# Optimization experiments

Hardware: AMD Instinct MI355X
Metric: run time of the kernel (lower is better)

## Reference

```python
import jax, jax.numpy as jnp
import numpy as np

N_NODES = 50000
N_EDGES = 800000
IN_FEATS = 64
HIDDEN = 32
HEADS = 8
NEG_SLOPE = 0.2


def gat_conv(x, W, a_l, a_r, b, src, dst, num_nodes):
    """DGL-style GATConv. x:[N,in], W:[in,H,O], a_l/a_r/b:[H,O]. Returns [N,H,O]."""
    feat = jnp.einsum('ni,iho->nho', x, W)              # [N,H,O]
    el = jnp.sum(feat * a_l, axis=-1)                   # [N,H]
    er = jnp.sum(feat * a_r, axis=-1)                   # [N,H]
    e = jax.nn.leaky_relu(el[src] + er[dst], NEG_SLOPE) # [E,H]
    # segment softmax over incoming edges of each dst node
    m = jax.ops.segment_max(e, dst, num_segments=num_nodes)   # [N,H]
    ex = jnp.exp(e - m[dst])                                   # [E,H]
    s = jax.ops.segment_sum(ex, dst, num_segments=num_nodes)   # [N,H]
    alpha = ex / s[dst]                                        # [E,H]
    out = jax.ops.segment_sum(feat[src] * alpha[:, :, None], dst,
                              num_segments=num_nodes)          # [N,H,O]
    return out + b


def setup_inputs() -> dict:
    key = jax.random.key(0)
    ks = jax.random.split(key, 12)
    g1 = 1.0 / np.sqrt(IN_FEATS)
    g2 = 1.0 / np.sqrt(HIDDEN * HEADS)
    return {
        'features': jax.random.normal(ks[0], (N_NODES, IN_FEATS), jnp.float32),
        'src': jax.random.randint(ks[1], (N_EDGES,), 0, N_NODES, jnp.int32),
        'dst': jax.random.randint(ks[2], (N_EDGES,), 0, N_NODES, jnp.int32),
        'edge_types': jax.random.randint(ks[3], (N_EDGES,), 0, 4, jnp.int32),
        'W1': jax.random.normal(ks[4], (IN_FEATS, HEADS, HIDDEN), jnp.float32) * g1,
        'al1': jax.random.normal(ks[5], (HEADS, HIDDEN), jnp.float32) * g1,
        'ar1': jax.random.normal(ks[6], (HEADS, HIDDEN), jnp.float32) * g1,
        'b1': jnp.zeros((HEADS, HIDDEN), jnp.float32),
        'W2': jax.random.normal(ks[7], (HIDDEN * HEADS, 1, 1), jnp.float32) * g2,
        'al2': jax.random.normal(ks[8], (1, 1), jnp.float32) * g2,
        'ar2': jax.random.normal(ks[9], (1, 1), jnp.float32) * g2,
        'b2': jnp.zeros((1, 1), jnp.float32),
    }


def reference(features, src, dst, edge_types, W1, al1, ar1, b1, W2, al2, ar2, b2):
    h = gat_conv(features, W1, al1, ar1, b1, src, dst, N_NODES)  # [N,H,O]
    h = jax.nn.relu(h.reshape(h.shape[0], -1))                   # [N,H*O]
    h = gat_conv(h, W2, al2, ar2, b2, src, dst, N_NODES)         # [N,1,1]
    h = jnp.squeeze(h, axis=1)                                   # [N,1]
    return jax.nn.sigmoid(h)
```

## Files before the change

### kernel.cpp

```cpp
#include <hip/hip_runtime.h>

#define N_NODES 50000
#define N_EDGES 800000
#define EDGE_BLOCKS 3125
#define CAP 64

typedef unsigned int uint32;
typedef unsigned short ushort16;
typedef unsigned char uchar8;
typedef short bf8v __attribute__((ext_vector_type(8)));
typedef float f32x4 __attribute__((ext_vector_type(4)));

__device__ __forceinline__ ushort16 f2bf(float f) {
  uint32 u = __float_as_uint(f);
  u += 0x7fffu + ((u >> 16) & 1u);
  return (ushort16)(u >> 16);
}

__global__ __launch_bounds__(256) void k_cvt_w1t(const float* __restrict__ W1,
    ushort16* __restrict__ w1t) {
  int t = threadIdx.x;
  int col = blockIdx.x * 4 + (t >> 6), k = t & 63;
  w1t[col * 64 + k] = f2bf(W1[k * 256 + col]);
}

__global__ __launch_bounds__(256) void k_build_feat(const float* __restrict__ x,
    const ushort16* __restrict__ w1t, const float* __restrict__ al1,
    const float* __restrict__ ar1, uchar8* __restrict__ feat8,
    float* __restrict__ el1, float* __restrict__ er1,
    const int* __restrict__ src, const int* __restrict__ dst,
    int* __restrict__ deg, int* __restrict__ esrc) {
  int t = threadIdx.x;
  if (blockIdx.x & 1) {
    int e = (blockIdx.x >> 1) * 256 + t;
    int d = dst[e];
    int p = atomicAdd(&deg[d], 1);
    if (p < CAP) esrc[d * CAP + p] = src[e];
    return;
  }
  int w = t >> 6, lane = t & 63;
  int quad = lane >> 4, m = lane & 15;
  int n0 = (blockIdx.x >> 1) * 16;
  const float* xr = x + (n0 + m) * 64 + quad * 8;
  float4 xa = *(const float4*)(xr);
  float4 xbv = *(const float4*)(xr + 4);
  float4 xc = *(const float4*)(xr + 32);
  float4 xd = *(const float4*)(xr + 36);
  bf8v a0, a1;
  a0[0] = (short)f2bf(xa.x); a0[1] = (short)f2bf(xa.y);
  a0[2] = (short)f2bf(xa.z); a0[3] = (short)f2bf(xa.w);
  a0[4] = (short)f2bf(xbv.x); a0[5] = (short)f2bf(xbv.y);
  a0[6] = (short)f2bf(xbv.z); a0[7] = (short)f2bf(xbv.w);
  a1[0] = (short)f2bf(xc.x); a1[1] = (short)f2bf(xc.y);
  a1[2] = (short)f2bf(xc.z); a1[3] = (short)f2bf(xc.w);
  a1[4] = (short)f2bf(xd.x); a1[5] = (short)f2bf(xd.y);
  a1[6] = (short)f2bf(xd.z); a1[7] = (short)f2bf(xd.w);
  float pl0[4] = {0.f, 0.f, 0.f, 0.f}, pr0[4] = {0.f, 0.f, 0.f, 0.f};
  float pl1[4] = {0.f, 0.f, 0.f, 0.f}, pr1[4] = {0.f, 0.f, 0.f, 0.f};
#pragma unroll
  for (int nt = 0; nt < 4; ++nt) {
    int colg = w * 64 + nt * 16 + m;
    const bf8v* bw = (const bf8v*)(w1t + colg * 64 + quad * 8);
    bf8v b0 = bw[0];
    bf8v b1 = bw[4];
    f32x4 acc = {0.f, 0.f, 0.f, 0.f};
    acc = __builtin_amdgcn_mfma_f32_16x16x32_bf16(a0, b0, acc, 0, 0, 0);
    acc = __builtin_amdgcn_mfma_f32_16x16x32_bf16(a1, b1, acc, 0, 0, 0);
    float al = al1[colg], ar = ar1[colg];
#pragma unroll
    for (int i = 0; i < 4; ++i) {
      uint32 pb = (uint32)__builtin_amdgcn_cvt_pk_fp8_f32(acc[i], acc[i], 0, 0);
      feat8[(size_t)(n0 + quad * 4 + i) * 256 + colg] = (uchar8)(pb & 0xffu);
      if (nt < 2) { pl0[i] += acc[i] * al; pr0[i] += acc[i] * ar; }
      else        { pl1[i] += acc[i] * al; pr1[i] += acc[i] * ar; }
    }
  }
#pragma unroll
  for (int off = 1; off < 16; off <<= 1) {
#pragma unroll
    for (int i = 0; i < 4; ++i) {
      pl0[i] += __shfl_xor(pl0[i], off, 64);
      pr0[i] += __shfl_xor(pr0[i], off, 64);
      pl1[i] += __shfl_xor(pl1[i], off, 64);
      pr1[i] += __shfl_xor(pr1[i], off, 64);
    }
  }
  if (m == 0) {
#pragma unroll
    for (int i = 0; i < 4; ++i) {
      int n = n0 + quad * 4 + i;
      el1[n * 8 + 2 * w] = pl0[i];
      er1[n * 8 + 2 * w] = pr0[i];
      el1[n * 8 + 2 * w + 1] = pl1[i];
      er1[n * 8 + 2 * w + 1] = pr1[i];
    }
  }
}

#define ACC8F8(u, ex)                                                    \
  {                                                                      \
    auto p0 = __builtin_amdgcn_cvt_pk_f32_fp8((u).x, 0);                 \
    auto p1 = __builtin_amdgcn_cvt_pk_f32_fp8((u).x, 1);                 \
    auto p2 = __builtin_amdgcn_cvt_pk_f32_fp8((u).y, 0);                 \
    auto p3 = __builtin_amdgcn_cvt_pk_f32_fp8((u).y, 1);                 \
    acc[0] += p0[0] * (ex); acc[1] += p0[1] * (ex);                      \
    acc[2] += p1[0] * (ex); acc[3] += p1[1] * (ex);                      \
    acc[4] += p2[0] * (ex); acc[5] += p2[1] * (ex);                      \
    acc[6] += p3[0] * (ex); acc[7] += p3[1] * (ex);                      \
  }

__global__ __launch_bounds__(256) void k_agg1(const int* __restrict__ deg,
    const int* __restrict__ esrc, const uint2* __restrict__ featv,
    const float* __restrict__ el1, const float* __restrict__ er1,
    const float* __restrict__ b1, const float* __restrict__ W2,
    float* __restrict__ feat2) {
  int t = threadIdx.x, nl = t >> 5, lt = t & 31;
  int n = blockIdx.x * 8 + nl;
  int h = lt >> 2;
  int begin = n * CAP;
  int d = deg[n]; d = d > CAP ? CAP : d;
  int end = begin + d;
  float er_h = er1[n * 8 + h];
  float acc[8] = {0.f, 0.f, 0.f, 0.f, 0.f, 0.f, 0.f, 0.f};
  float s = 0.f;
  int e = begin;
  for (; e + 8 <= end; e += 8) {
    int sn[8];
    uint2 u[8];
    float ex[8];
#pragma unroll
    for (int j = 0; j < 8; ++j) sn[j] = esrc[e + j];
#pragma unroll
    for (int j = 0; j < 8; ++j) u[j] = featv[sn[j] * 32 + lt];
#pragma unroll
    for (int j = 0; j < 8; ++j) {
      float v = el1[sn[j] * 8 + h] + er_h;
      v = v > 0.f ? v : 0.2f * v;
      ex[j] = __expf(v);
      s += ex[j];
    }
#pragma unroll
    for (int j = 0; j < 8; ++j) ACC8F8(u[j], ex[j]);
  }
  for (; e + 4 <= end; e += 4) {
    int sn[4];
    uint2 u[4];
    float ex[4];
#pragma unroll
    for (int j = 0; j < 4; ++j) sn[j] = esrc[e + j];
#pragma unroll
    for (int j = 0; j < 4; ++j) u[j] = featv[sn[j] * 32 + lt];
#pragma unroll
    for (int j = 0; j < 4; ++j) {
      float v = el1[sn[j] * 8 + h] + er_h;
      v = v > 0.f ? v : 0.2f * v;
      ex[j] = __expf(v);
      s += ex[j];
    }
#pragma unroll
    for (int j = 0; j < 4; ++j) ACC8F8(u[j], ex[j]);
  }
  for (; e < end; ++e) {
    int s0 = esrc[e];
    uint2 u0 = featv[s0 * 32 + lt];
    float v0 = el1[s0 * 8 + h] + er_h;
    v0 = v0 > 0.f ? v0 : 0.2f * v0;
    float ex0 = __expf(v0);
    s += ex0;
    ACC8F8(u0, ex0);
  }
  float inv = (d > 0) ? 1.f / s : 0.f;
  int o = lt * 8;
  float4 bb0 = *(const float4*)(b1 + o), bb1 = *(const float4*)(b1 + o + 4);
  float4 ww0 = *(const float4*)(W2 + o), ww1 = *(const float4*)(W2 + o + 4);
  float r = fmaxf(acc[0] * inv + bb0.x, 0.f) * ww0.x
          + fmaxf(acc[1] * inv + bb0.y, 0.f) * ww0.y
          + fmaxf(acc[2] * inv + bb0.z, 0.f) * ww0.z
          + fmaxf(acc[3] * inv + bb0.w, 0.f) * ww0.w
          + fmaxf(acc[4] * inv + bb1.x, 0.f) * ww1.x
          + fmaxf(acc[5] * inv + bb1.y, 0.f) * ww1.y
          + fmaxf(acc[6] * inv + bb1.z, 0.f) * ww1.z
          + fmaxf(acc[7] * inv + bb1.w, 0.f) * ww1.w;
  __shared__ float red[256];
  red[t] = r;
  __syncthreads();
  for (int off = 16; off > 0; off >>= 1) {
    if (lt < off) red[t] += red[t + off];
    __syncthreads();
  }
  if (lt == 0) feat2[n] = red[t];
}

__global__ __launch_bounds__(256) void k_layer2(const int* __restrict__ deg,
    const int* __restrict__ esrc, const float* __restrict__ feat2,
    const float* __restrict__ al2, const float* __restrict__ ar2,
    const float* __restrict__ b2, float* __restrict__ out) {
  int t = threadIdx.x, g = t >> 4, lt = t & 15;
  int n = blockIdx.x * 16 + g;
  int begin = n * CAP;
  int d = deg[n]; d = d > CAP ? CAP : d;
  int end = begin + d;
  float a2 = al2[0];
  float er_n = feat2[n] * ar2[0];
  float num = 0.f, s = 0.f;
  for (int e = begin + lt; e < end; e += 16) {
    int sN = esrc[e];
    float f = feat2[sN];
    float v = f * a2 + er_n;
    v = v > 0.f ? v : 0.2f * v;
    float ex = __expf(v);
    num += f * ex;
    s += ex;
  }
#pragma unroll
  for (int off = 8; off > 0; off >>= 1) {
    num += __shfl_down(num, off, 16);
    s += __shfl_down(s, off, 16);
  }
  if (lt == 0) {
    float val = (d > 0) ? num / s : 0.f;
    out[n] = 1.f / (1.f + __expf(-(val + b2[0])));
  }
}

extern "C" void kernel_launch(void* const* d_in, const int* in_sizes, int n_in,
                              void* d_out, int out_size, void* d_ws, size_t ws_size,
                              hipStream_t stream) {
  const float* x   = (const float*)d_in[0];
  const int* src   = (const int*)d_in[1];
  const int* dst   = (const int*)d_in[2];
  const float* W1  = (const float*)d_in[4];
  const float* al1 = (const float*)d_in[5];
  const float* ar1 = (const float*)d_in[6];
  const float* b1  = (const float*)d_in[7];
  const float* W2  = (const float*)d_in[8];
  const float* al2 = (const float*)d_in[9];
  const float* ar2 = (const float*)d_in[10];
  const float* b2  = (const float*)d_in[11];

  float* ws    = (float*)d_ws;
  float* el1   = ws;
  float* er1   = ws + 400000;
  float* feat2 = ws + 800000;
  int* deg     = (int*)ws + 850000;
  int* esrc    = (int*)ws + 900000;
  ushort16* w1t  = (ushort16*)((int*)ws + 4100000);
  uchar8* feat8  = (uchar8*)((int*)ws + 4108192);

  hipMemsetAsync(deg, 0, 50000 * sizeof(int), stream);

  k_cvt_w1t<<<64, 256, 0, stream>>>(W1, w1t);
  k_build_feat<<<EDGE_BLOCKS * 2, 256, 0, stream>>>(x, w1t, al1, ar1, feat8, el1, er1,
                                                    src, dst, deg, esrc);
  k_agg1<<<N_NODES / 8, 256, 0, stream>>>(deg, esrc, (const uint2*)feat8,
                                          el1, er1, b1, W2, feat2);
  k_layer2<<<N_NODES / 16, 256, 0, stream>>>(deg, esrc, feat2, al2, ar2, b2,
                                             (float*)d_out);
}
```

Baseline: 176.3 us.

## Store edge source indices as 16-bit, fold degree memset into init kernel

Edge source indices in the per-destination bucket array are stored as unsigned 16-bit values instead of int32, which halves the bucket footprint and lets the aggregation loop fetch 8 indices with one 16-byte load. The separate memset of the degree array is folded into the weight-transpose kernel, removing one launch. The scatter blocks now handle two edges per thread and are interleaved 1:2 with the feature blocks. Node ids go up to 49999, which still fits in 16 bits, but the layout would break for graphs with more than 65535 nodes.

```diff
diff --git a/kernel.cpp b/kernel.cpp
--- a/kernel.cpp
+++ b/kernel.cpp
@@ -2,7 +2,8 @@
 
 #define N_NODES 50000
 #define N_EDGES 800000
-#define EDGE_BLOCKS 3125
+#define FEAT_BLOCKS 3125
+#define SCAT_BLOCKS 1563
 #define CAP 64
 
 typedef unsigned int uint32;
@@ -17,11 +18,16 @@
   return (ushort16)(u >> 16);
 }
 
-__global__ __launch_bounds__(256) void k_cvt_w1t(const float* __restrict__ W1,
-    ushort16* __restrict__ w1t) {
-  int t = threadIdx.x;
-  int col = blockIdx.x * 4 + (t >> 6), k = t & 63;
-  w1t[col * 64 + k] = f2bf(W1[k * 256 + col]);
+__global__ __launch_bounds__(256) void k_init(const float* __restrict__ W1,
+    ushort16* __restrict__ w1t, int4* __restrict__ deg4) {
+  int b = blockIdx.x, t = threadIdx.x;
+  if (b < 64) {
+    int col = b * 4 + (t >> 6), k = t & 63;
+    w1t[col * 64 + k] = f2bf(W1[k * 256 + col]);
+  } else {
+    int i = (b - 64) * 256 + t;
+    if (i < 12500) deg4[i] = make_int4(0, 0, 0, 0);
+  }
 }
 
 __global__ __launch_bounds__(256) void k_build_feat(const float* __restrict__ x,
@@ -29,18 +35,31 @@
     const float* __restrict__ ar1, uchar8* __restrict__ feat8,
     float* __restrict__ el1, float* __restrict__ er1,
     const int* __restrict__ src, const int* __restrict__ dst,
-    int* __restrict__ deg, int* __restrict__ esrc) {
+    int* __restrict__ deg, unsigned short* __restrict__ esrc16) {
   int t = threadIdx.x;
-  if (blockIdx.x & 1) {
-    int e = (blockIdx.x >> 1) * 256 + t;
-    int d = dst[e];
-    int p = atomicAdd(&deg[d], 1);
-    if (p < CAP) esrc[d * CAP + p] = src[e];
+  int r3 = blockIdx.x % 3;
+  if (r3 == 2) {
+    int e0 = (blockIdx.x / 3) * 512 + t;
+    int e1 = e0 + 256;
+    if (e0 < N_EDGES) {
+      int d0 = dst[e0];
+      int s0 = src[e0];
+      int p0 = atomicAdd(&deg[d0], 1);
+      if (p0 < CAP) esrc16[d0 * CAP + p0] = (unsigned short)s0;
+    }
+    if (e1 < N_EDGES) {
+      int d1 = dst[e1];
+      int s1 = src[e1];
+      int p1 = atomicAdd(&deg[d1], 1);
+      if (p1 < CAP) esrc16[d1 * CAP + p1] = (unsigned short)s1;
+    }
     return;
   }
+  int fidx = (blockIdx.x / 3) * 2 + r3;
+  if (fidx >= FEAT_BLOCKS) return;
   int w = t >> 6, lane = t & 63;
   int quad = lane >> 4, m = lane & 15;
-  int n0 = (blockIdx.x >> 1) * 16;
+  int n0 = fidx * 16;
   const float* xr = x + (n0 + m) * 64 + quad * 8;
   float4 xa = *(const float4*)(xr);
   float4 xbv = *(const float4*)(xr + 4);
@@ -110,7 +129,7 @@
   }
 
 __global__ __launch_bounds__(256) void k_agg1(const int* __restrict__ deg,
-    const int* __restrict__ esrc, const uint2* __restrict__ featv,
+    const unsigned short* __restrict__ esrc16, const uint2* __restrict__ featv,
     const float* __restrict__ el1, const float* __restrict__ er1,
     const float* __restrict__ b1, const float* __restrict__ W2,
     float* __restrict__ feat2) {
@@ -125,11 +144,13 @@
   float s = 0.f;
   int e = begin;
   for (; e + 8 <= end; e += 8) {
-    int sn[8];
+    uint4 sv = *(const uint4*)(esrc16 + e);
+    int sn[8] = {(int)(sv.x & 0xffffu), (int)(sv.x >> 16),
+                 (int)(sv.y & 0xffffu), (int)(sv.y >> 16),
+                 (int)(sv.z & 0xffffu), (int)(sv.z >> 16),
+                 (int)(sv.w & 0xffffu), (int)(sv.w >> 16)};
     uint2 u[8];
     float ex[8];
-#pragma unroll
-    for (int j = 0; j < 8; ++j) sn[j] = esrc[e + j];
 #pragma unroll
     for (int j = 0; j < 8; ++j) u[j] = featv[sn[j] * 32 + lt];
 #pragma unroll
@@ -147,7 +168,7 @@
     uint2 u[4];
     float ex[4];
 #pragma unroll
-    for (int j = 0; j < 4; ++j) sn[j] = esrc[e + j];
+    for (int j = 0; j < 4; ++j) sn[j] = (int)esrc16[e + j];
 #pragma unroll
     for (int j = 0; j < 4; ++j) u[j] = featv[sn[j] * 32 + lt];
 #pragma unroll
@@ -161,7 +182,7 @@
     for (int j = 0; j < 4; ++j) ACC8F8(u[j], ex[j]);
   }
   for (; e < end; ++e) {
-    int s0 = esrc[e];
+    int s0 = (int)esrc16[e];
     uint2 u0 = featv[s0 * 32 + lt];
     float v0 = el1[s0 * 8 + h] + er_h;
     v0 = v0 > 0.f ? v0 : 0.2f * v0;
@@ -192,7 +213,7 @@
 }
 
 __global__ __launch_bounds__(256) void k_layer2(const int* __restrict__ deg,
-    const int* __restrict__ esrc, const float* __restrict__ feat2,
+    const unsigned short* __restrict__ esrc16, const float* __restrict__ feat2,
     const float* __restrict__ al2, const float* __restrict__ ar2,
     const float* __restrict__ b2, float* __restrict__ out) {
   int t = threadIdx.x, g = t >> 4, lt = t & 15;
@@ -204,7 +225,7 @@
   float er_n = feat2[n] * ar2[0];
   float num = 0.f, s = 0.f;
   for (int e = begin + lt; e < end; e += 16) {
-    int sN = esrc[e];
+    int sN = (int)esrc16[e];
     float f = feat2[sN];
     float v = f * a2 + er_n;
     v = v > 0.f ? v : 0.2f * v;
@@ -243,17 +264,15 @@
   float* er1   = ws + 400000;
   float* feat2 = ws + 800000;
   int* deg     = (int*)ws + 850000;
-  int* esrc    = (int*)ws + 900000;
-  ushort16* w1t  = (ushort16*)((int*)ws + 4100000);
-  uchar8* feat8  = (uchar8*)((int*)ws + 4108192);
-
-  hipMemsetAsync(deg, 0, 50000 * sizeof(int), stream);
-
-  k_cvt_w1t<<<64, 256, 0, stream>>>(W1, w1t);
-  k_build_feat<<<EDGE_BLOCKS * 2, 256, 0, stream>>>(x, w1t, al1, ar1, feat8, el1, er1,
-                                                    src, dst, deg, esrc);
-  k_agg1<<<N_NODES / 8, 256, 0, stream>>>(deg, esrc, (const uint2*)feat8,
+  unsigned short* esrc16 = (unsigned short*)((int*)ws + 900000);
+  ushort16* w1t  = (ushort16*)((int*)ws + 2500000);
+  uchar8* feat8  = (uchar8*)((int*)ws + 2508192);
+
+  k_init<<<64 + 49, 256, 0, stream>>>(W1, w1t, (int4*)deg);
+  k_build_feat<<<FEAT_BLOCKS + SCAT_BLOCKS + 1, 256, 0, stream>>>(
+      x, w1t, al1, ar1, feat8, el1, er1, src, dst, deg, esrc16);
+  k_agg1<<<N_NODES / 8, 256, 0, stream>>>(deg, esrc16, (const uint2*)feat8,
                                           el1, er1, b1, W2, feat2);
-  k_layer2<<<N_NODES / 16, 256, 0, stream>>>(deg, esrc, feat2, al2, ar2, b2,
+  k_layer2<<<N_NODES / 16, 256, 0, stream>>>(deg, esrc16, feat2, al2, ar2, b2,
                                              (float*)d_out);
 }
```

Measured after the change: 170.8 us. -3.1%, faster.
